# Kernel tuning notes

Measured on AMD Instinct MI355X. Metric: run time of the kernel, lower is better.

The kernel has to match this reference:

```python
import jax, jax.numpy as jnp
import numpy as np

B, T, F, H, S, E, L = 64, 256, 80, 512, 512, 512, 3


def setup_inputs() -> dict:
    key = jax.random.key(0)
    ks = jax.random.split(key, 16)
    sc = 0.05  # keep LSTM gates in a sane range
    inp = {
        "padded_targets": jax.random.normal(ks[0], (B, T, F), jnp.float32),
        "encoder_out": jax.random.normal(ks[1], (B, S, E), jnp.float32),
        "input_seq_lens": jax.random.randint(ks[2], (B,), S // 2, S + 1, jnp.int32),
        "Wih0": jax.random.normal(ks[3], (4 * H, F + E), jnp.float32) * sc,
        "Whh0": jax.random.normal(ks[4], (4 * H, H), jnp.float32) * sc,
        "b0": jax.random.normal(ks[5], (4 * H,), jnp.float32) * sc,
        "Wih1": jax.random.normal(ks[6], (4 * H, H), jnp.float32) * sc,
        "Whh1": jax.random.normal(ks[7], (4 * H, H), jnp.float32) * sc,
        "b1": jax.random.normal(ks[8], (4 * H,), jnp.float32) * sc,
        "Wih2": jax.random.normal(ks[9], (4 * H, H), jnp.float32) * sc,
        "Whh2": jax.random.normal(ks[10], (4 * H, H), jnp.float32) * sc,
        "b2": jax.random.normal(ks[11], (4 * H,), jnp.float32) * sc,
        "Wq": jax.random.normal(ks[12], (H, E), jnp.float32) * sc,
        "Wfc": jax.random.normal(ks[13], (E, F), jnp.float32) * sc,
        "bfc": jax.random.normal(ks[14], (F,), jnp.float32) * sc,
    }
    return inp


def _lstm_cell(x, h, c, Wih, Whh, b):
    g = x @ Wih.T + h @ Whh.T + b                      # [B, 4H]
    i, f, gg, o = jnp.split(g, 4, axis=-1)             # PyTorch gate order i,f,g,o
    c_new = jax.nn.sigmoid(f) * c + jax.nn.sigmoid(i) * jnp.tanh(gg)
    h_new = jax.nn.sigmoid(o) * jnp.tanh(c_new)
    return h_new, c_new


def _decode(padded_targets, encoder_out, mask_bias, params):
    (Wih0, Whh0, b0, Wih1, Whh1, b1, Wih2, Whh2, b2, Wq, Wfc, bfc) = params
    Wihs = (Wih0, Wih1, Wih2)
    Whhs = (Whh0, Whh1, Whh2)
    bs = (b0, b1, b2)
    scale = 1.0 / jnp.sqrt(jnp.asarray(E, jnp.float32))

    def step(carry, xt):
        hs, cs, ctx = carry                            # hs/cs: tuples of [B,H]; ctx [B,E]
        inp = jnp.concatenate([xt, ctx], axis=1)       # [B, F+E]  (teach=1.0 -> always target)
        new_h, new_c = [], []
        for l in range(L):
            hl, cl = _lstm_cell(inp, hs[l], cs[l], Wihs[l], Whhs[l], bs[l])
            new_h.append(hl)
            new_c.append(cl)
            inp = hl
        q = new_h[-1] @ Wq                             # [B,E]
        scores = jnp.einsum('be,bse->bs', q, encoder_out) * scale + mask_bias
        w = jax.nn.softmax(scores, axis=-1)            # [B,S]
        ctx_new = jnp.einsum('bs,bse->be', w, encoder_out)
        pred = ctx_new @ Wfc + bfc                     # [B,F]
        return (tuple(new_h), tuple(new_c), ctx_new), pred

    h0 = tuple(jnp.zeros((B, H), padded_targets.dtype) for _ in range(L))
    c0 = tuple(jnp.zeros((B, H), padded_targets.dtype) for _ in range(L))
    ctx0 = jnp.zeros((B, E), padded_targets.dtype)
    xs = jnp.swapaxes(padded_targets[:, :-1], 0, 1)    # [T-1, B, F]
    _, preds = jax.lax.scan(step, (h0, c0, ctx0), xs)
    return jnp.swapaxes(preds, 0, 1)                   # [B, T-1, F]


def reference(padded_targets, encoder_out, input_seq_lens,
              Wih0, Whh0, b0, Wih1, Whh1, b1, Wih2, Whh2, b2, Wq, Wfc, bfc):
    valid = jnp.arange(S)[None, :] < input_seq_lens[:, None]     # [B,S]
    mask_bias = jnp.where(valid, 0.0, -1e9).astype(jnp.float32)
    params = (Wih0, Whh0, b0, Wih1, Whh1, b1, Wih2, Whh2, b2, Wq, Wfc, bfc)
    return _decode(padded_targets, encoder_out, mask_bias, params)
```

## Files before the change

kernel.cpp:

```cpp
#include <hip/hip_runtime.h>

#define NBLK 256
#define NTHR 512

typedef float f32x4 __attribute__((ext_vector_type(4)));
typedef unsigned int u32;

__device__ __forceinline__ float sigm(float x){ return 1.f/(1.f+__expf(-x)); }
__device__ __forceinline__ float tanh_(float x){ return 1.f - 2.f/(__expf(2.f*x)+1.f); }

__device__ __forceinline__ float wred_sum(float v){
  #pragma unroll
  for (int off=32; off; off>>=1) v += __shfl_xor(v, off, 64);
  return v;
}

__device__ __forceinline__ u32 cvtpk(float lo, float hi){
  u32 r; asm("v_cvt_pk_bf16_f32 %0,%1,%2":"=v"(r):"v"(lo),"v"(hi)); return r;
}
__device__ __forceinline__ float bflo(u32 u){ return __uint_as_float(u<<16); }
__device__ __forceinline__ float bfhi(u32 u){ return __uint_as_float(u & 0xFFFF0000u); }

__device__ __forceinline__ void st_sys(float* p, float v){
  __hip_atomic_store(p, v, __ATOMIC_RELAXED, __HIP_MEMORY_SCOPE_AGENT);
}
__device__ __forceinline__ void st_sysu(u32* p, u32 v){
  __hip_atomic_store(p, v, __ATOMIC_RELAXED, __HIP_MEMORY_SCOPE_AGENT);
}
__device__ __forceinline__ float ald(const float* p){
  return __hip_atomic_load(p, __ATOMIC_RELAXED, __HIP_MEMORY_SCOPE_AGENT);
}
__device__ __forceinline__ u32 aldu(const u32* p){
  return __hip_atomic_load(p, __ATOMIC_RELAXED, __HIP_MEMORY_SCOPE_AGENT);
}

__device__ __forceinline__ void vmwait0(){
  asm volatile("s_waitcnt vmcnt(0)" ::: "memory");
  __builtin_amdgcn_sched_barrier(0);
}
__device__ __forceinline__ void lgkm0(){
  asm volatile("s_waitcnt lgkmcnt(0)" ::: "memory");
  __builtin_amdgcn_sched_barrier(0);
}

__device__ __forceinline__ void gsync(unsigned* bar, int w, unsigned& ep){
  ++ep;
  __builtin_amdgcn_s_waitcnt(0);
  __syncthreads();
  if (threadIdx.x == 0){
    const int g = w >> 4;
    const unsigned epoch = ep;
    bool rootfin = false;
    unsigned o = __hip_atomic_fetch_add(bar + g*32, 1u, __ATOMIC_ACQ_REL, __HIP_MEMORY_SCOPE_AGENT);
    if (o == 15u){
      __hip_atomic_store(bar + g*32, 0u, __ATOMIC_RELAXED, __HIP_MEMORY_SCOPE_AGENT);
      unsigned o2 = __hip_atomic_fetch_add(bar + 16*32, 1u, __ATOMIC_ACQ_REL, __HIP_MEMORY_SCOPE_AGENT);
      if (o2 == 15u){
        __hip_atomic_store(bar + 16*32, 0u, __ATOMIC_RELAXED, __HIP_MEMORY_SCOPE_AGENT);
        __hip_atomic_store(bar + 17*32, epoch, __ATOMIC_RELEASE, __HIP_MEMORY_SCOPE_AGENT);
        rootfin = true;
      }
    }
    if ((w & 15) == 0){
      if (!rootfin){
        while (__hip_atomic_load(bar + 17*32, __ATOMIC_RELAXED, __HIP_MEMORY_SCOPE_AGENT) < epoch)
          __builtin_amdgcn_s_sleep(1);
      }
      __hip_atomic_store(bar + (18+g)*32, epoch, __ATOMIC_RELEASE, __HIP_MEMORY_SCOPE_AGENT);
    } else {
      while (__hip_atomic_load(bar + (18+g)*32, __ATOMIC_RELAXED, __HIP_MEMORY_SCOPE_AGENT) < epoch)
        __builtin_amdgcn_s_sleep(1);
    }
  }
  __syncthreads();
}


template<bool L0T>
__device__ __forceinline__ void lstm_layer(
    int w, int tid, const float (&wt)[8][2], const float (&wx)[4], float br,
    const u32* __restrict__ inu, float* sc_c,
    u32* __restrict__ dstA, int strA,
    u32* __restrict__ dstB, int strB,
    u32* stage, float* scr, u32* xsu, float* sG4,
    const float* __restrict__ tgt, int t)
{
  const int lane = tid & 63, r = tid >> 6;

  if (L0T){
    #pragma unroll
    for (int i=0;i<5;++i){
      const int flat = tid + (i<<9);
      const int row = flat/40, col = flat - row*40;
      const float* q = tgt + ((row<<8)+t)*80 + (col<<1);
      xsu[flat] = cvtpk(q[0], q[1]);
    }
  }
  uint4 ld[16];
  #pragma unroll
  for (int i=0;i<16;++i){
    const u32* p = inu + (i<<11) + (tid<<2);
    asm volatile("global_load_dwordx4 %0, %1, off sc0 sc1" : "=v"(ld[i]) : "v"(p));
  }
  vmwait0();
  #pragma unroll
  for (int i=0;i<16;++i) *(uint4*)(stage + (i<<11) + (tid<<2)) = ld[i];
  __syncthreads();

  float* sw = scr + r*512;
  #pragma unroll 1
  for (int ch=0; ch<8; ++ch){
    float pv[8];
    #pragma unroll
    for (int bb=0; bb<8; ++bb){
      const u32* rowp = stage + ((ch<<3)+bb)*512 + lane;
      float a0=0.f,a1=0.f,a2=0.f,a3=0.f;
      #pragma unroll
      for (int i=0;i<8;i+=2){
        const u32 e0 = rowp[(i<<6)];
        const u32 e1 = rowp[((i+1)<<6)];
        a0 = fmaf(wt[i][0],   bflo(e0), a0);
        a1 = fmaf(wt[i][1],   bfhi(e0), a1);
        a2 = fmaf(wt[i+1][0], bflo(e1), a2);
        a3 = fmaf(wt[i+1][1], bfhi(e1), a3);
      }
      if (L0T && lane < 20){
        const u32 x0 = xsu[((ch<<3)+bb)*40 + (lane<<1)];
        const u32 x1 = xsu[((ch<<3)+bb)*40 + (lane<<1) + 1];
        a0 = fmaf(wx[0], bflo(x0), a0);
        a1 = fmaf(wx[1], bfhi(x0), a1);
        a2 = fmaf(wx[2], bflo(x1), a2);
        a3 = fmaf(wx[3], bfhi(x1), a3);
      }
      pv[bb] = (a0+a1)+(a2+a3);
    }
    #pragma unroll
    for (int bb=0; bb<8; ++bb) sw[(bb<<6) + lane] = pv[bb];
    lgkm0();
    {
      const int bb2 = lane>>3, m = lane&7;
      const float* pp = sw + (bb2<<6) + (m<<3);
      float v = ((pp[0]+pp[1])+(pp[2]+pp[3])) + ((pp[4]+pp[5])+(pp[6]+pp[7]));
      v += __shfl_xor(v,1,64);
      v += __shfl_xor(v,2,64);
      v += __shfl_xor(v,4,64);
      if (m==0) sG4[((ch<<3)+bb2)*8 + r] = v + br;
    }
  }
  lgkm0();
  __syncthreads();

  if (tid < 128){
    const int b = tid>>1, jl = tid&1;
    const float* g = sG4 + b*8 + (jl<<2);
    const float gi = sigm(g[0]), gf = sigm(g[1]);
    const float gg = tanh_(g[2]), go = sigm(g[3]);
    const float cn = gf*sc_c[tid] + gi*gg;
    sc_c[tid] = cn;
    const float hn = go*tanh_(cn);
    const float hn1 = __shfl(hn, tid^1, 64);
    if (!(tid&1)){
      const u32 hp = cvtpk(hn, hn1);
      st_sysu(dstA + b*strA, hp);
      st_sysu(dstB + b*strB, hp);
    }
  }
}

#define ZERO_U   212992
#define FP_OFF   212992
#define ENC_OFF  475648
#define ENC_CNT  8388608

__global__ __launch_bounds__(NTHR, 2)
void sd_kernel(const float* __restrict__ tgt,  const float* __restrict__ enc,
               const int*   __restrict__ lens,
               const float* __restrict__ Wih0, const float* __restrict__ Whh0, const float* __restrict__ b0v,
               const float* __restrict__ Wih1, const float* __restrict__ Whh1, const float* __restrict__ b1v,
               const float* __restrict__ Wih2, const float* __restrict__ Whh2, const float* __restrict__ b2v,
               const float* __restrict__ Wq,   const float* __restrict__ Wfc,  const float* __restrict__ bfc,
               float* __restrict__ out, void* __restrict__ wsv, int ebf)
{
  unsigned* bar = (unsigned*)wsv;
  u32* wsu = (u32*)((char*)wsv + 8192);
  u32* IN0u = wsu;
  u32* IN1u = wsu + 65536;
  u32* IN2u = wsu + 131072;
  u32* H2u  = wsu + 196608;
  float* F  = (float*)(wsu + FP_OFF);
  float* QP = F;
  float* PC = F + 131072;
  float* MS = F + 262144;
  u32* encbfu = wsu + ENC_OFF;

  const int w = blockIdx.x, tid = threadIdx.x;
  const int lane = tid & 63, r = tid >> 6;
  unsigned ep = 0;

  __shared__ __attribute__((aligned(16))) u32 SM[40320];
  u32*   stage = SM;
  float* scr   = (float*)(SM + 32768);
  u32*   xsu   = SM + 36864;
  float* sG4   = (float*)(SM + 39424);
  float* sc_c  = (float*)(SM + 39936);
  float* sBig   = (float*)SM;
  float* sVec   = (float*)(SM + 4096);
  float* sSmall = (float*)(SM + 4608);

  const int wrow = ((r&3)<<9) + (w<<1) + (r>>2);
  float w0r[8][2], w1r[8][2], w2r[8][2], wx0[4];
  #pragma unroll
  for (int i=0;i<8;++i){
    const int k = 2*(lane + (i<<6));
    if (k < 512){
      w0r[i][0] = Wih0[wrow*592 + 80 + k];
      w0r[i][1] = Wih0[wrow*592 + 80 + k + 1];
      w1r[i][0] = Wih1[(wrow<<9) + k];
      w1r[i][1] = Wih1[(wrow<<9) + k + 1];
      w2r[i][0] = Wih2[(wrow<<9) + k];
      w2r[i][1] = Wih2[(wrow<<9) + k + 1];
    } else {
      w0r[i][0] = Whh0[(wrow<<9) + k - 512];
      w0r[i][1] = Whh0[(wrow<<9) + k - 511];
      w1r[i][0] = Whh1[(wrow<<9) + k - 512];
      w1r[i][1] = Whh1[(wrow<<9) + k - 511];
      w2r[i][0] = Whh2[(wrow<<9) + k - 512];
      w2r[i][1] = Whh2[(wrow<<9) + k - 511];
    }
  }
  #pragma unroll
  for (int m=0;m<4;++m)
    wx0[m] = (lane < 20) ? Wih0[wrow*592 + (lane<<2) + m] : 0.f;
  const float br0 = b0v[wrow], br1 = b1v[wrow], br2 = b2v[wrow];

  if (tid < 384) sc_c[tid] = 0.f;
  for (int i = w*NTHR + tid; i < ZERO_U; i += NBLK*NTHR) st_sysu(wsu + i, 0u);
  if (ebf){
    for (int i = w*NTHR + tid; i < ENC_CNT; i += NBLK*NTHR)
      st_sysu(encbfu + i, cvtpk(enc[2*i], enc[2*i+1]));
  }
  gsync(bar, w, ep);

  for (int t=0; t<255; ++t){
    const int p = t & 1, np = p ^ 1;
    u32* IN0p = IN0u + p*32768;  u32* IN0n = IN0u + np*32768;
    u32* IN1p = IN1u + p*32768;  u32* IN1n = IN1u + np*32768;
    u32* IN2p = IN2u + p*32768;  u32* IN2n = IN2u + np*32768;

    lstm_layer<true >(w,tid, w0r, wx0, br0, IN0p, sc_c,
                      IN0n+256+w, 512, IN1p+w, 512, stage,scr,xsu,sG4, tgt, t);
    gsync(bar,w,ep);
    lstm_layer<false>(w,tid, w1r, wx0, br1, IN1p, sc_c+128,
                      IN1n+256+w, 512, IN2p+w, 512, stage,scr,xsu,sG4, tgt, t);
    gsync(bar,w,ep);
    lstm_layer<false>(w,tid, w2r, wx0, br2, IN2p, sc_c+256,
                      IN2n+256+w, 512, H2u+w, 256, stage,scr,xsu,sG4, tgt, t);
    gsync(bar,w,ep);

    {
      const int b = w & 63, kq = w >> 6;
      if (tid < 64){
        const u32 u = aldu(H2u + b*256 + kq*64 + tid);
        sVec[2*tid]   = bflo(u);
        sVec[2*tid+1] = bfhi(u);
      }
      __syncthreads();
      const float* wqp = Wq + ((size_t)(kq<<7)<<9) + tid;
      float acc = 0.f;
      #pragma unroll 4
      for (int k=0;k<128;++k) acc = fmaf(sVec[k], wqp[(size_t)k<<9], acc);
      st_sys(&QP[(((kq<<6)+b)<<9) + tid], acc);
    }
    gsync(bar,w,ep);

    {
      const int b = w & 63, sq = w >> 6;
      const int len  = lens[b];
      const int wv = tid >> 6;
      sVec[tid] = ald(&QP[(b<<9)+tid]) + ald(&QP[((64+b)<<9)+tid])
                + ald(&QP[((128+b)<<9)+tid]) + ald(&QP[((192+b)<<9)+tid]);
      __syncthreads();
      const float4 qA = *(const float4*)(sVec + (lane<<3));
      const float4 qB = *(const float4*)(sVec + (lane<<3) + 4);
      float mr = -3.0e38f, lr = 0.f;
      float c0=0,c1=0,c2=0,c3=0,c4=0,c5=0,c6=0,c7=0;
      const float scale = 0.04419417382415922f;
      if (ebf){
        const u32* ebase = encbfu + (((size_t)b)<<17) + (lane<<2);
        #pragma unroll 1
        for (int rr=0; rr<16; ++rr){
          const int srow = (sq<<7) + (wv<<4) + rr;
          if (srow >= len) break;
          const uint4 eu = *(const uint4*)(ebase + ((size_t)srow<<8));
          const float e0=bflo(eu.x), e1=bfhi(eu.x), e2=bflo(eu.y), e3=bfhi(eu.y);
          const float e4=bflo(eu.z), e5=bfhi(eu.z), e6=bflo(eu.w), e7=bfhi(eu.w);
          float d0 = qA.x*e0, d1 = qA.y*e1, d2 = qA.z*e2, d3 = qA.w*e3;
          d0 = fmaf(qB.x, e4, d0); d1 = fmaf(qB.y, e5, d1);
          d2 = fmaf(qB.z, e6, d2); d3 = fmaf(qB.w, e7, d3);
          float d = wred_sum((d0+d1)+(d2+d3));
          const float sc = d*scale;
          const float mn = fmaxf(mr, sc);
          const float sf = __expf(mr - mn);
          const float pe = __expf(sc - mn);
          lr = fmaf(lr, sf, pe);
          c0 = fmaf(c0, sf, pe*e0); c1 = fmaf(c1, sf, pe*e1);
          c2 = fmaf(c2, sf, pe*e2); c3 = fmaf(c3, sf, pe*e3);
          c4 = fmaf(c4, sf, pe*e4); c5 = fmaf(c5, sf, pe*e5);
          c6 = fmaf(c6, sf, pe*e6); c7 = fmaf(c7, sf, pe*e7);
          mr = mn;
        }
      } else {
        #pragma unroll 1
        for (int rr=0; rr<16; ++rr){
          const int srow = (sq<<7) + (wv<<4) + rr;
          if (srow >= len) break;
          const float* ep2 = enc + (((size_t)(b<<9)+srow)<<9) + (lane<<3);
          const float4 e0v = *(const float4*)(ep2);
          const float4 e1v = *(const float4*)(ep2+4);
          float d0 = qA.x*e0v.x, d1 = qA.y*e0v.y, d2 = qA.z*e0v.z, d3 = qA.w*e0v.w;
          d0 = fmaf(qB.x, e1v.x, d0); d1 = fmaf(qB.y, e1v.y, d1);
          d2 = fmaf(qB.z, e1v.z, d2); d3 = fmaf(qB.w, e1v.w, d3);
          float d = wred_sum((d0+d1)+(d2+d3));
          const float sc = d*scale;
          const float mn = fmaxf(mr, sc);
          const float sf = __expf(mr - mn);
          const float pe = __expf(sc - mn);
          lr = fmaf(lr, sf, pe);
          c0 = fmaf(c0, sf, pe*e0v.x); c1 = fmaf(c1, sf, pe*e0v.y);
          c2 = fmaf(c2, sf, pe*e0v.z); c3 = fmaf(c3, sf, pe*e0v.w);
          c4 = fmaf(c4, sf, pe*e1v.x); c5 = fmaf(c5, sf, pe*e1v.y);
          c6 = fmaf(c6, sf, pe*e1v.z); c7 = fmaf(c7, sf, pe*e1v.w);
          mr = mn;
        }
      }
      if (lane==0){ sSmall[wv] = mr; sSmall[8+wv] = lr; }
      {
        float4 v0 = {c0,c1,c2,c3}, v1 = {c4,c5,c6,c7};
        *(float4*)(sBig + (wv<<9) + (lane<<3))     = v0;
        *(float4*)(sBig + (wv<<9) + (lane<<3) + 4) = v1;
      }
      __syncthreads();
      float M = sSmall[0];
      #pragma unroll
      for (int i=1;i<8;++i) M = fmaxf(M, sSmall[i]);
      float L = 0.f, acc = 0.f;
      #pragma unroll
      for (int i=0;i<8;++i){
        const float A = __expf(sSmall[i]-M);
        L   = fmaf(A, sSmall[8+i], L);
        acc = fmaf(A, sBig[(i<<9)+tid], acc);
      }
      st_sys(&PC[(((sq<<6)+b)<<9)+tid], acc);
      if (tid==0){
        st_sys(&MS[(((sq<<6)+b)<<1)],   M);
        st_sys(&MS[(((sq<<6)+b)<<1)+1], L);
      }
    }
    gsync(bar,w,ep);

    if (w < 64){
      const int b = w;
      const float m0 = ald(&MS[(b)<<1]),      S0 = ald(&MS[((b)<<1)+1]);
      const float m1 = ald(&MS[(64+b)<<1]),   S1 = ald(&MS[((64+b)<<1)+1]);
      const float m2 = ald(&MS[(128+b)<<1]),  S2 = ald(&MS[((128+b)<<1)+1]);
      const float m3 = ald(&MS[(192+b)<<1]),  S3 = ald(&MS[((192+b)<<1)+1]);
      const float M  = fmaxf(fmaxf(m0,m1), fmaxf(m2,m3));
      const float a0=__expf(m0-M), a1=__expf(m1-M), a2=__expf(m2-M), a3=__expf(m3-M);
      const float inv = 1.f/(a0*S0 + a1*S1 + a2*S2 + a3*S3);
      const float c = (a0*ald(&PC[(b<<9)+tid])       + a1*ald(&PC[((64+b)<<9)+tid])
                     + a2*ald(&PC[((128+b)<<9)+tid]) + a3*ald(&PC[((192+b)<<9)+tid])) * inv;
      const float c1 = __shfl(c, tid^1, 64);
      if (!(tid&1)) st_sysu(IN0n + b*512 + (tid>>1), cvtpk(c, c1));
      sVec[tid] = c;
      __syncthreads();
      if (tid < 80){
        float acc = 0.f;
        #pragma unroll 4
        for (int e2=0;e2<512;++e2) acc = fmaf(sVec[e2], Wfc[e2*80+tid], acc);
        out[((size_t)b*255 + t)*80 + tid] = acc + bfc[tid];
      }
    }
    gsync(bar,w,ep);
  }
}

extern "C" void kernel_launch(void* const* d_in, const int* in_sizes, int n_in,
                              void* d_out, int out_size, void* d_ws, size_t ws_size,
                              hipStream_t stream) {
  const float* tgt  = (const float*)d_in[0];
  const float* enc  = (const float*)d_in[1];
  const int*   lens = (const int*)  d_in[2];
  const float* Wih0 = (const float*)d_in[3];
  const float* Whh0 = (const float*)d_in[4];
  const float* b0   = (const float*)d_in[5];
  const float* Wih1 = (const float*)d_in[6];
  const float* Whh1 = (const float*)d_in[7];
  const float* b1   = (const float*)d_in[8];
  const float* Wih2 = (const float*)d_in[9];
  const float* Whh2 = (const float*)d_in[10];
  const float* b2   = (const float*)d_in[11];
  const float* Wq   = (const float*)d_in[12];
  const float* Wfc  = (const float*)d_in[13];
  const float* bfc  = (const float*)d_in[14];

  const size_t need = 8192ull + ((size_t)ENC_OFF + (size_t)ENC_CNT)*4ull;
  const int ebf = (ws_size >= need) ? 1 : 0;

  hipMemsetAsync(d_ws, 0, 8192, stream);
  sd_kernel<<<NBLK, NTHR, 0, stream>>>(tgt, enc, lens,
                                       Wih0, Whh0, b0,
                                       Wih1, Whh1, b1,
                                       Wih2, Whh2, b2,
                                       Wq, Wfc, bfc,
                                       (float*)d_out, d_ws, ebf);
}
```

Baseline: 33.35 ms.

## Split LSTM work across batch halves with two gate rows per block

Each block now handles two hidden units (four gate rows each) for half of the batch (32 rows), instead of one unit for the full batch. Every staged input element is reused against two weight rows held in registers, and each block stages half as much input into LDS per layer. The aim is to halve the per-block global-to-LDS traffic and the number of LDS reads per FMA. The cost is doubled weight registers, which may raise register pressure and reduce occupancy.

```diff
diff --git a/kernel.cpp b/kernel.cpp
--- a/kernel.cpp
+++ b/kernel.cpp
@@ -78,7 +78,9 @@
 
 template<bool L0T>
 __device__ __forceinline__ void lstm_layer(
-    int w, int tid, const float (&wt)[8][2], const float (&wx)[4], float br,
+    int jt, int bt, int tid,
+    const float (&wt)[2][8][2], const float (&wx)[2][4],
+    float brA, float brB,
     const u32* __restrict__ inu, float* sc_c,
     u32* __restrict__ dstA, int strA,
     u32* __restrict__ dstB, int strB,
@@ -86,73 +88,91 @@
     const float* __restrict__ tgt, int t)
 {
   const int lane = tid & 63, r = tid >> 6;
+  const u32* src = inu + bt*16384;
 
   if (L0T){
     #pragma unroll
-    for (int i=0;i<5;++i){
+    for (int i=0;i<3;++i){
       const int flat = tid + (i<<9);
-      const int row = flat/40, col = flat - row*40;
-      const float* q = tgt + ((row<<8)+t)*80 + (col<<1);
-      xsu[flat] = cvtpk(q[0], q[1]);
-    }
-  }
-  uint4 ld[16];
+      if (flat < 1280){
+        const int row = flat/40, col = flat - row*40;
+        const float* q = tgt + ((((bt<<5)+row)<<8) + t)*80 + (col<<1);
+        xsu[flat] = cvtpk(q[0], q[1]);
+      }
+    }
+  }
+  uint4 ld[8];
   #pragma unroll
-  for (int i=0;i<16;++i){
-    const u32* p = inu + (i<<11) + (tid<<2);
+  for (int i=0;i<8;++i){
+    const u32* p = src + (i<<11) + (tid<<2);
     asm volatile("global_load_dwordx4 %0, %1, off sc0 sc1" : "=v"(ld[i]) : "v"(p));
   }
   vmwait0();
   #pragma unroll
-  for (int i=0;i<16;++i) *(uint4*)(stage + (i<<11) + (tid<<2)) = ld[i];
+  for (int i=0;i<8;++i) *(uint4*)(stage + (i<<11) + (tid<<2)) = ld[i];
   __syncthreads();
 
-  float* sw = scr + r*512;
+  float* sw = scr + r*1024;
   #pragma unroll 1
-  for (int ch=0; ch<8; ++ch){
-    float pv[8];
+  for (int ch=0; ch<4; ++ch){
+    float pv0[8], pv1[8];
     #pragma unroll
     for (int bb=0; bb<8; ++bb){
       const u32* rowp = stage + ((ch<<3)+bb)*512 + lane;
-      float a0=0.f,a1=0.f,a2=0.f,a3=0.f;
+      float a0=0.f,a1=0.f,a2=0.f,a3=0.f, c0=0.f,c1=0.f,c2=0.f,c3=0.f;
       #pragma unroll
       for (int i=0;i<8;i+=2){
         const u32 e0 = rowp[(i<<6)];
         const u32 e1 = rowp[((i+1)<<6)];
-        a0 = fmaf(wt[i][0],   bflo(e0), a0);
-        a1 = fmaf(wt[i][1],   bfhi(e0), a1);
-        a2 = fmaf(wt[i+1][0], bflo(e1), a2);
-        a3 = fmaf(wt[i+1][1], bfhi(e1), a3);
+        const float f0=bflo(e0), f1=bfhi(e0), f2=bflo(e1), f3=bfhi(e1);
+        a0 = fmaf(wt[0][i][0],   f0, a0);
+        a1 = fmaf(wt[0][i][1],   f1, a1);
+        a2 = fmaf(wt[0][i+1][0], f2, a2);
+        a3 = fmaf(wt[0][i+1][1], f3, a3);
+        c0 = fmaf(wt[1][i][0],   f0, c0);
+        c1 = fmaf(wt[1][i][1],   f1, c1);
+        c2 = fmaf(wt[1][i+1][0], f2, c2);
+        c3 = fmaf(wt[1][i+1][1], f3, c3);
       }
       if (L0T && lane < 20){
-        const u32 x0 = xsu[((ch<<3)+bb)*40 + (lane<<1)];
-        const u32 x1 = xsu[((ch<<3)+bb)*40 + (lane<<1) + 1];
-        a0 = fmaf(wx[0], bflo(x0), a0);
-        a1 = fmaf(wx[1], bfhi(x0), a1);
-        a2 = fmaf(wx[2], bflo(x1), a2);
-        a3 = fmaf(wx[3], bfhi(x1), a3);
-      }
-      pv[bb] = (a0+a1)+(a2+a3);
+        const int lrow = (ch<<3)+bb;
+        const u32 x0 = xsu[lrow*40 + (lane<<1)];
+        const u32 x1 = xsu[lrow*40 + (lane<<1) + 1];
+        const float g0=bflo(x0), g1=bfhi(x0), g2=bflo(x1), g3=bfhi(x1);
+        a0 = fmaf(wx[0][0], g0, a0); a1 = fmaf(wx[0][1], g1, a1);
+        a2 = fmaf(wx[0][2], g2, a2); a3 = fmaf(wx[0][3], g3, a3);
+        c0 = fmaf(wx[1][0], g0, c0); c1 = fmaf(wx[1][1], g1, c1);
+        c2 = fmaf(wx[1][2], g2, c2); c3 = fmaf(wx[1][3], g3, c3);
+      }
+      pv0[bb] = (a0+a1)+(a2+a3);
+      pv1[bb] = (c0+c1)+(c2+c3);
     }
     #pragma unroll
-    for (int bb=0; bb<8; ++bb) sw[(bb<<6) + lane] = pv[bb];
+    for (int bb=0; bb<8; ++bb){
+      sw[(bb<<6) + lane]       = pv0[bb];
+      sw[512 + (bb<<6) + lane] = pv1[bb];
+    }
     lgkm0();
     {
       const int bb2 = lane>>3, m = lane&7;
       const float* pp = sw + (bb2<<6) + (m<<3);
-      float v = ((pp[0]+pp[1])+(pp[2]+pp[3])) + ((pp[4]+pp[5])+(pp[6]+pp[7]));
-      v += __shfl_xor(v,1,64);
-      v += __shfl_xor(v,2,64);
-      v += __shfl_xor(v,4,64);
-      if (m==0) sG4[((ch<<3)+bb2)*8 + r] = v + br;
+      float v0 = ((pp[0]+pp[1])+(pp[2]+pp[3])) + ((pp[4]+pp[5])+(pp[6]+pp[7]));
+      const float* pq = pp + 512;
+      float v1 = ((pq[0]+pq[1])+(pq[2]+pq[3])) + ((pq[4]+pq[5])+(pq[6]+pq[7]));
+      v0 += __shfl_xor(v0,1,64); v0 += __shfl_xor(v0,2,64); v0 += __shfl_xor(v0,4,64);
+      v1 += __shfl_xor(v1,1,64); v1 += __shfl_xor(v1,2,64); v1 += __shfl_xor(v1,4,64);
+      if (m==0){
+        sG4[(((ch<<3)+bb2)<<4) + r]     = v0 + brA;
+        sG4[(((ch<<3)+bb2)<<4) + r + 8] = v1 + brB;
+      }
     }
   }
   lgkm0();
   __syncthreads();
 
   if (tid < 128){
-    const int b = tid>>1, jl = tid&1;
-    const float* g = sG4 + b*8 + (jl<<2);
+    const int b = tid>>2, jl = tid&3;
+    const float* g = sG4 + (b<<4) + (jl<<2);
     const float gi = sigm(g[0]), gf = sigm(g[1]);
     const float gg = tanh_(g[2]), go = sigm(g[3]);
     const float cn = gf*sc_c[tid] + gi*gg;
@@ -161,8 +181,10 @@
     const float hn1 = __shfl(hn, tid^1, 64);
     if (!(tid&1)){
       const u32 hp = cvtpk(hn, hn1);
-      st_sysu(dstA + b*strA, hp);
-      st_sysu(dstB + b*strB, hp);
+      const int gb = (bt<<5) + b;
+      const int col = (jt<<1) + (jl>>1);
+      st_sysu(dstA + gb*strA + col, hp);
+      st_sysu(dstB + gb*strB + col, hp);
     }
   }
 }
@@ -195,43 +217,45 @@
 
   const int w = blockIdx.x, tid = threadIdx.x;
   const int lane = tid & 63, r = tid >> 6;
+  const int jt = w >> 1, bt = w & 1;
   unsigned ep = 0;
 
-  __shared__ __attribute__((aligned(16))) u32 SM[40320];
+  __shared__ __attribute__((aligned(16))) u32 SM[26752];
   u32*   stage = SM;
-  float* scr   = (float*)(SM + 32768);
-  u32*   xsu   = SM + 36864;
-  float* sG4   = (float*)(SM + 39424);
-  float* sc_c  = (float*)(SM + 39936);
+  float* scr   = (float*)(SM + 16384);
+  u32*   xsu   = SM + 24576;
+  float* sG4   = (float*)(SM + 25856);
+  float* sc_c  = (float*)(SM + 26368);
   float* sBig   = (float*)SM;
   float* sVec   = (float*)(SM + 4096);
   float* sSmall = (float*)(SM + 4608);
 
-  const int wrow = ((r&3)<<9) + (w<<1) + (r>>2);
-  float w0r[8][2], w1r[8][2], w2r[8][2], wx0[4];
+  const int wrowA = ((r&3)<<9) + (jt<<2) + (r>>2);
+  const int wrowB = wrowA + 2;
+  float w0r[2][8][2], w1r[2][8][2], w2r[2][8][2], wx0[2][4];
   #pragma unroll
-  for (int i=0;i<8;++i){
-    const int k = 2*(lane + (i<<6));
-    if (k < 512){
-      w0r[i][0] = Wih0[wrow*592 + 80 + k];
-      w0r[i][1] = Wih0[wrow*592 + 80 + k + 1];
-      w1r[i][0] = Wih1[(wrow<<9) + k];
-      w1r[i][1] = Wih1[(wrow<<9) + k + 1];
-      w2r[i][0] = Wih2[(wrow<<9) + k];
-      w2r[i][1] = Wih2[(wrow<<9) + k + 1];
-    } else {
-      w0r[i][0] = Whh0[(wrow<<9) + k - 512];
-      w0r[i][1] = Whh0[(wrow<<9) + k - 511];
-      w1r[i][0] = Whh1[(wrow<<9) + k - 512];
-      w1r[i][1] = Whh1[(wrow<<9) + k - 511];
-      w2r[i][0] = Whh2[(wrow<<9) + k - 512];
-      w2r[i][1] = Whh2[(wrow<<9) + k - 511];
-    }
-  }
-  #pragma unroll
-  for (int m=0;m<4;++m)
-    wx0[m] = (lane < 20) ? Wih0[wrow*592 + (lane<<2) + m] : 0.f;
-  const float br0 = b0v[wrow], br1 = b1v[wrow], br2 = b2v[wrow];
+  for (int s=0;s<2;++s){
+    const int wr = s ? wrowB : wrowA;
+    #pragma unroll
+    for (int i=0;i<8;++i){
+      const int k = 2*(lane + (i<<6));
+      if (k < 512){
+        w0r[s][i][0] = Wih0[wr*592 + 80 + k];   w0r[s][i][1] = Wih0[wr*592 + 81 + k];
+        w1r[s][i][0] = Wih1[(wr<<9) + k];       w1r[s][i][1] = Wih1[(wr<<9) + k + 1];
+        w2r[s][i][0] = Wih2[(wr<<9) + k];       w2r[s][i][1] = Wih2[(wr<<9) + k + 1];
+      } else {
+        w0r[s][i][0] = Whh0[(wr<<9) + k - 512]; w0r[s][i][1] = Whh0[(wr<<9) + k - 511];
+        w1r[s][i][0] = Whh1[(wr<<9) + k - 512]; w1r[s][i][1] = Whh1[(wr<<9) + k - 511];
+        w2r[s][i][0] = Whh2[(wr<<9) + k - 512]; w2r[s][i][1] = Whh2[(wr<<9) + k - 511];
+      }
+    }
+    #pragma unroll
+    for (int m=0;m<4;++m)
+      wx0[s][m] = (lane < 20) ? Wih0[wr*592 + (lane<<2) + m] : 0.f;
+  }
+  const float br0A=b0v[wrowA], br0B=b0v[wrowB];
+  const float br1A=b1v[wrowA], br1B=b1v[wrowB];
+  const float br2A=b2v[wrowA], br2B=b2v[wrowB];
 
   if (tid < 384) sc_c[tid] = 0.f;
   for (int i = w*NTHR + tid; i < ZERO_U; i += NBLK*NTHR) st_sysu(wsu + i, 0u);
@@ -247,14 +271,14 @@
     u32* IN1p = IN1u + p*32768;  u32* IN1n = IN1u + np*32768;
     u32* IN2p = IN2u + p*32768;  u32* IN2n = IN2u + np*32768;
 
-    lstm_layer<true >(w,tid, w0r, wx0, br0, IN0p, sc_c,
-                      IN0n+256+w, 512, IN1p+w, 512, stage,scr,xsu,sG4, tgt, t);
-    gsync(bar,w,ep);
-    lstm_layer<false>(w,tid, w1r, wx0, br1, IN1p, sc_c+128,
-                      IN1n+256+w, 512, IN2p+w, 512, stage,scr,xsu,sG4, tgt, t);
-    gsync(bar,w,ep);
-    lstm_layer<false>(w,tid, w2r, wx0, br2, IN2p, sc_c+256,
-                      IN2n+256+w, 512, H2u+w, 256, stage,scr,xsu,sG4, tgt, t);
+    lstm_layer<true >(jt,bt,tid, w0r, wx0, br0A, br0B, IN0p, sc_c,
+                      IN0n+256, 512, IN1p, 512, stage,scr,xsu,sG4, tgt, t);
+    gsync(bar,w,ep);
+    lstm_layer<false>(jt,bt,tid, w1r, wx0, br1A, br1B, IN1p, sc_c+128,
+                      IN1n+256, 512, IN2p, 512, stage,scr,xsu,sG4, tgt, t);
+    gsync(bar,w,ep);
+    lstm_layer<false>(jt,bt,tid, w2r, wx0, br2A, br2B, IN2p, sc_c+256,
+                      IN2n+256, 512, H2u, 256, stage,scr,xsu,sG4, tgt, t);
     gsync(bar,w,ep);
 
     {
```

Result: faster. 30.51 ms (-8.5%).
